# Kernel optimization log

Hardware: AMD Instinct MI355X
Metric: run time of the kernel (lower is better)

The kernel has to match this reference:

```python
import jax, jax.numpy as jnp
import numpy as np

V = 100000   # vocab (emb_size == stoich_size so all 8 branches index safely)
D = 256      # emb_dimension
S = 128      # stoich_dimension
H = 512      # hidden_size
B = 8192     # batch of skip-gram pairs
K = 32       # negative samples per pair
NUM_REGULAR = 60000  # num_regular_words


def _mlp(x, w1, b1, w2, b2):
    # Sequential(Linear(S,H), ReLU, Linear(H,D))
    return jax.nn.relu(x @ w1 + b1) @ w2 + b2


def setup_inputs() -> dict:
    key = jax.random.key(0)
    k = jax.random.split(key, 14)
    initrange = 1.0 / D
    return {
        "pos_u": jax.random.randint(k[0], (B,), 0, V),
        "pos_v": jax.random.randint(k[1], (B,), 0, V),
        "neg_v": jax.random.randint(k[2], (B, K), 0, V),
        "u_emb": jax.random.uniform(k[3], (V, D), jnp.float32, -initrange, initrange),
        "v_emb": jax.random.normal(k[4], (V, D), jnp.float32) * 0.01,
        "stoich": jax.random.uniform(k[5], (V, S), jnp.float32),
        "tw1": jax.random.normal(k[6], (S, H), jnp.float32) * 0.05,
        "tb1": jnp.zeros((H,), jnp.float32),
        "tw2": jax.random.normal(k[7], (H, D), jnp.float32) * 0.05,
        "tb2": jnp.zeros((D,), jnp.float32),
        "cw1": jax.random.normal(k[8], (S, H), jnp.float32) * 0.05,
        "cb1": jnp.zeros((H,), jnp.float32),
        "cw2": jax.random.normal(k[9], (H, D), jnp.float32) * 0.05,
        "cb2": jnp.zeros((D,), jnp.float32),
    }


def _masked_score(emb_u, emb_v, emb_neg_v, u_mask, v_mask, neg_v_mask):
    # pos: [B]
    pos = jnp.clip(jnp.sum(emb_u * emb_v, axis=1), -10.0, 10.0)
    pos = jnp.where(v_mask, 0.0, -jax.nn.log_sigmoid(pos))
    # neg: [B,K] = bmm(emb_neg_v [B,K,D], emb_u [B,D,1])
    neg = jnp.clip(jnp.einsum("bkd,bd->bk", emb_neg_v, emb_u), -10.0, 10.0)
    ls = jnp.where(neg_v_mask, 0.0, jax.nn.log_sigmoid(-neg))
    neg_score = -jnp.sum(ls, axis=1)
    return jnp.where(u_mask, 0.0, pos + neg_score)


def reference(pos_u, pos_v, neg_v, u_emb, v_emb, stoich,
              tw1, tb1, tw2, tb2, cw1, cb1, cw2, cb2):
    emb_u_w = u_emb[pos_u]                 # [B,D]
    emb_v_w = v_emb[pos_v]                 # [B,D]
    emb_neg_v_w = v_emb[neg_v]             # [B,K,D]
    emb_u_m = _mlp(stoich[pos_u], tw1, tb1, tw2, tb2)       # [B,D]
    emb_v_m = _mlp(stoich[pos_v], cw1, cb1, cw2, cb2)       # [B,D]
    emb_neg_v_m = _mlp(stoich[neg_v], cw1, cb1, cw2, cb2)   # [B,K,D]

    u_pairs = [(emb_u_w, pos_u >= NUM_REGULAR), (emb_u_m, pos_u < NUM_REGULAR)]
    v_pairs = [(emb_v_w, pos_v >= NUM_REGULAR), (emb_v_m, pos_v < NUM_REGULAR)]
    n_pairs = [(emb_neg_v_w, neg_v >= NUM_REGULAR), (emb_neg_v_m, neg_v < NUM_REGULAR)]

    total = jnp.zeros((B,), emb_u_w.dtype)
    for eu, um in u_pairs:
        for ev, vm in v_pairs:
            for env, nm in n_pairs:
                total = total + _masked_score(eu, ev, env, um, vm, nm)
    return jnp.mean(total)
```

## Files before the change

kernel.cpp:

```cpp
#include <hip/hip_runtime.h>
#include <hip/hip_bf16.h>
#include <math.h>

#define V_SIZE 100000
#define D_DIM  256
#define S_DIM  128
#define H_DIM  512
#define B_SIZE 8192
#define K_NEG  32
#define NR     60000
#define NMOD   (V_SIZE - NR)

#define TM     48
#define CBLK   834
#define UBLK   171
#define MC_PAD (CBLK * TM)
#define MU_PAD (UBLK * TM)
#define HPAD   516

typedef __attribute__((ext_vector_type(8))) short bf16x8;
typedef __attribute__((ext_vector_type(8))) unsigned short u16x8;
typedef __attribute__((ext_vector_type(4))) float f32x4;

static __device__ __forceinline__ short f2bf(float f) {
    unsigned u = __builtin_bit_cast(unsigned, f);
    unsigned r = (u + 0x7fffu + ((u >> 16) & 1u)) >> 16;
    return (short)r;
}
static __device__ __forceinline__ float bf2f(unsigned short h) {
    return __builtin_bit_cast(float, ((unsigned)h) << 16);
}


#define N_VC   (NR * D_DIM / 4)
#define N_CONV (MC_PAD * S_DIM / 4)
#define N_XU   (MU_PAD * S_DIM / 4)
#define N_TR   393216

__global__ __launch_bounds__(256) void prep_kernel(
    const float* __restrict__ stoich, const int* __restrict__ pos_u,
    const float* __restrict__ v_emb,
    const float* __restrict__ tw1, const float* __restrict__ cw1,
    const float* __restrict__ tw2, const float* __restrict__ cw2,
    short* __restrict__ vall,
    short* __restrict__ xc, short* __restrict__ xu,
    short* __restrict__ W1T_t, short* __restrict__ W1T_c,
    short* __restrict__ W2T_t, short* __restrict__ W2T_c)
{
    int t = blockIdx.x * 256 + threadIdx.x;
    if (t < N_VC) {
        int r  = t >> 6;
        int fr = t & 15;
        int wv = (t & 63) >> 4;
        const float* rp = v_emb + (size_t)r * D_DIM + wv * 64 + fr;
        short4 o;
        o.x = f2bf(rp[0]); o.y = f2bf(rp[16]); o.z = f2bf(rp[32]); o.w = f2bf(rp[48]);
        ((short4*)vall)[t] = o;
        return;
    }
    t -= N_VC;
    if (t < N_CONV + N_XU) {
        const bool cside = t < N_CONV;
        const int e    = (cside ? t : t - N_CONV) * 4;
        const int j0   = e & 7;
        const int lane = (e >> 3) & 63;
        const int ks   = (e >> 9) & 3;
        const int rt   = e >> 11;
        const int row  = rt * 16 + (lane & 15);
        const int k    = ks * 32 + (lane >> 4) * 8 + j0;
        short4 o = {0, 0, 0, 0};
        if (cside) {
            if (row < NMOD) {
                const float4 v = *(const float4*)(stoich + (size_t)(NR + row) * S_DIM + k);
                o.x = f2bf(v.x); o.y = f2bf(v.y); o.z = f2bf(v.z); o.w = f2bf(v.w);
            }
            ((short4*)xc)[t] = o;
        } else {
            if (row < B_SIZE) {
                int pu = pos_u[row];
                const float4 v = *(const float4*)(stoich + (size_t)pu * S_DIM + k);
                o.x = f2bf(v.x); o.y = f2bf(v.y); o.z = f2bf(v.z); o.w = f2bf(v.w);
            }
            ((short4*)xu)[t - N_CONV] = o;
        }
    } else {
        int t3 = t - (N_CONV + N_XU);
        if (t3 < 131072) {
            const float* src = (t3 < 65536) ? tw1 : cw1;
            short*       dst = (t3 < 65536) ? W1T_t : W1T_c;
            int t4 = t3 & 65535;
            int j = t4 & 7, lane = (t4 >> 3) & 63;
            int nt = (t4 >> 9) & 31, ks = (t4 >> 14) & 3;
            int k = ks * 32 + (lane >> 4) * 8 + j, n = nt * 16 + (lane & 15);
            dst[t4] = f2bf(src[(size_t)k * H_DIM + n]);
        } else {
            int t5 = t3 - 131072;
            const float* src = (t5 < 131072) ? tw2 : cw2;
            short*       dst = (t5 < 131072) ? W2T_t : W2T_c;
            int t4 = t5 & 131071;
            int j = t4 & 7, lane = (t4 >> 3) & 63;
            int nt = (t4 >> 9) & 15, ks = (t4 >> 13) & 15;
            int k = ks * 32 + (lane >> 4) * 8 + j, n = nt * 16 + (lane & 15);
            dst[t4] = f2bf(src[(size_t)k * D_DIM + n]);
        }
    }
}

__global__ __launch_bounds__(256, 3) void fused_mlp_kernel(
    const short* __restrict__ Xc,  const short* __restrict__ W1c,
    const float* __restrict__ b1c, const short* __restrict__ W2c,
    const float* __restrict__ b2c, short* __restrict__ outc,
    const short* __restrict__ Xu,  const short* __restrict__ W1u,
    const float* __restrict__ b1u, const short* __restrict__ W2u,
    const float* __restrict__ b2u, short* __restrict__ outu)
{
    __shared__ short sH[TM * HPAD];

    const int blk = blockIdx.x;
    const short *A, *W1T, *W2T; const float *b1, *b2; short* out;
    int m0, rtb;
    if (blk < CBLK) { A = Xc; W1T = W1c; b1 = b1c; W2T = W2c; b2 = b2c;
                      out = outc; m0 = blk * TM; rtb = blk * 3; }
    else            { A = Xu; W1T = W1u; b1 = b1u; W2T = W2u; b2 = b2u;
                      out = outu; m0 = (blk - CBLK) * TM; rtb = (blk - CBLK) * 3; }

    const int lane = threadIdx.x & 63;
    const int wv   = threadIdx.x >> 6;
    const int fr   = lane & 15;
    const int q    = lane >> 4;

    const short* Ap = A + (size_t)rtb * 2048 + lane * 8;
    bf16x8 af[4][3];
    #pragma unroll
    for (int ks = 0; ks < 4; ++ks)
        #pragma unroll
        for (int mi = 0; mi < 3; ++mi)
            af[ks][mi] = *(const bf16x8*)(Ap + mi * 2048 + ks * 512);

    #pragma unroll
    for (int half = 0; half < 2; ++half) {
        const int nt0 = wv * 8 + half * 4;
        const short* Bp = W1T + (size_t)nt0 * 512 + lane * 8;
        f32x4 acc[3][4] = {};
        #pragma unroll
        for (int ks = 0; ks < 4; ++ks) {
            bf16x8 bfr[4];
            #pragma unroll
            for (int ni = 0; ni < 4; ++ni)
                bfr[ni] = *(const bf16x8*)(Bp + ks * 16384 + ni * 512);
            #pragma unroll
            for (int mi = 0; mi < 3; ++mi)
                #pragma unroll
                for (int ni = 0; ni < 4; ++ni)
                    acc[mi][ni] = __builtin_amdgcn_mfma_f32_16x16x32_bf16(
                        af[ks][mi], bfr[ni], acc[mi][ni], 0, 0, 0);
        }
        #pragma unroll
        for (int ni = 0; ni < 4; ++ni) {
            int c = (nt0 + ni) * 16 + fr;
            float bv = b1[c];
            #pragma unroll
            for (int mi = 0; mi < 3; ++mi)
                #pragma unroll
                for (int r = 0; r < 4; ++r)
                    sH[(mi * 16 + q * 4 + r) * HPAD + c] =
                        f2bf(fmaxf(acc[mi][ni][r] + bv, 0.f));
        }
    }

    const short* Bp2 = W2T + (size_t)(wv * 4) * 512 + lane * 8;
    f32x4 acc2[3][4] = {};
    bf16x8 bA[4], bB[4], bC[4], bD[4], aA[3], aB[3];

    #define LOAD_B(ks, dst)                                                   \
        _Pragma("unroll")                                                     \
        for (int ni = 0; ni < 4; ++ni)                                        \
            dst[ni] = *(const bf16x8*)(Bp2 + (ks) * 8192 + ni * 512);
    #define LOAD_A(ks, dst)                                                   \
        _Pragma("unroll")                                                     \
        for (int mi = 0; mi < 3; ++mi) {                                      \
            const short* hp = &sH[(mi * 16 + fr) * HPAD + (ks) * 32 + q * 8]; \
            short4 lo = *(const short4*)hp;                                   \
            short4 hi = *(const short4*)(hp + 4);                             \
            bf16x8 v;                                                         \
            v[0] = lo.x; v[1] = lo.y; v[2] = lo.z; v[3] = lo.w;               \
            v[4] = hi.x; v[5] = hi.y; v[6] = hi.z; v[7] = hi.w;               \
            dst[mi] = v;                                                      \
        }

    LOAD_B(0, bA);
    LOAD_B(1, bB);
    LOAD_B(2, bC);
    __syncthreads();
    LOAD_A(0, aA);
    #pragma unroll
    for (int ks = 0; ks < 16; ++ks) {
        if (ks < 13) { LOAD_B(ks + 3, bD); }
        if (ks < 15) { LOAD_A(ks + 1, aB); }
        #pragma unroll
        for (int mi = 0; mi < 3; ++mi)
            #pragma unroll
            for (int ni = 0; ni < 4; ++ni)
                acc2[mi][ni] = __builtin_amdgcn_mfma_f32_16x16x32_bf16(
                    aA[mi], bA[ni], acc2[mi][ni], 0, 0, 0);
        if (ks < 15) {
            #pragma unroll
            for (int i = 0; i < 4; ++i) { bA[i] = bB[i]; bB[i] = bC[i]; bC[i] = bD[i]; }
            #pragma unroll
            for (int i = 0; i < 3; ++i) aA[i] = aB[i];
        }
    }
    #undef LOAD_A
    #undef LOAD_B

    float bv[4];
    #pragma unroll
    for (int ni = 0; ni < 4; ++ni)
        bv[ni] = b2[wv * 64 + ni * 16 + fr];
    #pragma unroll
    for (int mi = 0; mi < 3; ++mi)
        #pragma unroll
        for (int r = 0; r < 4; ++r) {
            int row = m0 + mi * 16 + q * 4 + r;
            short4 s;
            s.x = f2bf(acc2[mi][0][r] + bv[0]);
            s.y = f2bf(acc2[mi][1][r] + bv[1]);
            s.z = f2bf(acc2[mi][2][r] + bv[2]);
            s.w = f2bf(acc2[mi][3][r] + bv[3]);
            *(short4*)(out + (size_t)row * D_DIM + wv * 64 + fr * 4) = s;
        }
}

__device__ __forceinline__ float logsig_fast(float x) {
    float t = __expf(-fabsf(x));
    return fminf(x, 0.f) - __logf(1.f + t);
}
__device__ __forceinline__ float clip10(float x) {
    return fminf(fmaxf(x, -10.f), 10.f);
}

__global__ __launch_bounds__(256) void score_kernel(
    const int*   __restrict__ pos_u,
    const int*   __restrict__ pos_v,
    const int*   __restrict__ neg_v,
    const float* __restrict__ u_emb,
    const unsigned short* __restrict__ Vall,
    const unsigned short* __restrict__ Ubuf,
    float* __restrict__ partials)
{
    const int b    = blockIdx.x;
    const int lane = threadIdx.x & 63;
    const int wv   = threadIdx.x >> 6;
    const int g    = lane >> 4;
    const int l    = lane & 15;
    const int w64  = (l >> 2) * 64;
    const int s4   = (l & 3) * 4;

    const int* nv = neg_v + (size_t)b * K_NEG + wv * 8;
    int ix0 = nv[g];
    int ix1 = nv[4 + g];
    const unsigned short* r0p = Vall + (size_t)ix0 * D_DIM + l * 16;
    const unsigned short* r1p = Vall + (size_t)ix1 * D_DIM + l * 16;
    u16x8 r0a = *(const u16x8*)r0p;
    u16x8 r0b = *(const u16x8*)(r0p + 8);
    u16x8 r1a = *(const u16x8*)r1p;
    u16x8 r1b = *(const u16x8*)(r1p + 8);
    u16x8 rpa, rpb;
    if (wv == 0) {
        const unsigned short* rpp = Vall + (size_t)pos_v[b] * D_DIM + l * 16;
        rpa = *(const u16x8*)rpp;
        rpb = *(const u16x8*)(rpp + 8);
    }

    float euf[16];
    int pu = pos_u[b];
    if (pu < NR) {
        const float* eup = u_emb + (size_t)pu * D_DIM;
        #pragma unroll
        for (int n = 0; n < 4; ++n) {
            float4 v = *(const float4*)(eup + w64 + n * 16 + s4);
            euf[0 + n] = v.x; euf[4 + n] = v.y; euf[8 + n] = v.z; euf[12 + n] = v.w;
        }
    } else {
        const unsigned short* eup = Ubuf + (size_t)b * D_DIM + l * 16;
        u16x8 h0 = *(const u16x8*)eup;
        u16x8 h1 = *(const u16x8*)(eup + 8);
        #pragma unroll
        for (int i = 0; i < 8; ++i) { euf[i] = bf2f(h0[i]); euf[8 + i] = bf2f(h1[i]); }
    }

    float part = 0.f;

    float d0 = 0.f, d1 = 0.f;
    #pragma unroll
    for (int i = 0; i < 8; ++i) {
        d0 += euf[i] * bf2f(r0a[i]) + euf[8 + i] * bf2f(r0b[i]);
        d1 += euf[i] * bf2f(r1a[i]) + euf[8 + i] * bf2f(r1b[i]);
    }
    #pragma unroll
    for (int o = 1; o < 16; o <<= 1) {
        d0 += __shfl_xor(d0, o, 64);
        d1 += __shfl_xor(d1, o, 64);
    }
    part -= logsig_fast(-clip10(d0));
    part -= logsig_fast(-clip10(d1));

    if (wv == 0) {
        float dp = 0.f;
        #pragma unroll
        for (int i = 0; i < 8; ++i)
            dp += euf[i] * bf2f(rpa[i]) + euf[8 + i] * bf2f(rpb[i]);
        #pragma unroll
        for (int o = 1; o < 16; o <<= 1) dp += __shfl_xor(dp, o, 64);
        if (g == 0) part -= logsig_fast(clip10(dp));
    }

    float ws = part;
    #pragma unroll
    for (int o = 32; o; o >>= 1) ws += __shfl_xor(ws, o, 64);
    __shared__ float sp[4];
    if (lane == 0) sp[wv] = ws * 0.0625f;
    __syncthreads();
    if (threadIdx.x == 0)
        partials[b] = sp[0] + sp[1] + sp[2] + sp[3];
}

__global__ __launch_bounds__(256) void reduce_kernel(
    const float* __restrict__ partials, float* __restrict__ out)
{
    float s = 0.f;
    for (int i = threadIdx.x; i < B_SIZE; i += 256) s += partials[i];
    #pragma unroll
    for (int o = 32; o; o >>= 1) s += __shfl_xor(s, o, 64);
    __shared__ float sp[4];
    if ((threadIdx.x & 63) == 0) sp[threadIdx.x >> 6] = s;
    __syncthreads();
    if (threadIdx.x == 0)
        out[0] = (sp[0] + sp[1] + sp[2] + sp[3]) * (2.0f / (float)B_SIZE);
}

extern "C" void kernel_launch(void* const* d_in, const int* in_sizes, int n_in,
                              void* d_out, int out_size, void* d_ws, size_t ws_size,
                              hipStream_t stream) {
    const int*   pos_u  = (const int*)  d_in[0];
    const int*   pos_v  = (const int*)  d_in[1];
    const int*   neg_v  = (const int*)  d_in[2];
    const float* u_emb  = (const float*)d_in[3];
    const float* v_emb  = (const float*)d_in[4];
    const float* stoich = (const float*)d_in[5];
    const float* tw1    = (const float*)d_in[6];
    const float* tb1    = (const float*)d_in[7];
    const float* tw2    = (const float*)d_in[8];
    const float* tb2    = (const float*)d_in[9];
    const float* cw1    = (const float*)d_in[10];
    const float* cb1    = (const float*)d_in[11];
    const float* cw2    = (const float*)d_in[12];
    const float* cb2    = (const float*)d_in[13];
    float* out = (float*)d_out;

    char* ws = (char*)d_ws;
    short* Xbf   = (short*)(ws);
    short* Xu    = (short*)(ws + 10248192);
    short* W1T_t = (short*)(ws + 12349440);
    short* W1T_c = (short*)(ws + 12480512);
    short* W2T_t = (short*)(ws + 12611584);
    short* W2T_c = (short*)(ws + 12873728);
    short* Vall  = (short*)(ws + 13135872);
    short* Ubuf  = (short*)(ws + 64352256);
    float* parts = (float*)(ws + 68554752);
    short* tab_c = Vall + (size_t)NR * D_DIM;

    dim3 blk(256);

    prep_kernel<<<dim3((N_VC + N_CONV + N_XU + N_TR) / 256), blk, 0, stream>>>(
        stoich, pos_u, v_emb, tw1, cw1, tw2, cw2,
        Vall, Xbf, Xu, W1T_t, W1T_c, W2T_t, W2T_c);

    fused_mlp_kernel<<<dim3(CBLK + UBLK), blk, 0, stream>>>(
        Xbf, W1T_c, cb1, W2T_c, cb2, tab_c,
        Xu,  W1T_t, tb1, W2T_t, tb2, Ubuf);

    score_kernel<<<dim3(B_SIZE), blk, 0, stream>>>(
        pos_u, pos_v, neg_v, u_emb,
        (const unsigned short*)Vall, (const unsigned short*)Ubuf, parts);
    reduce_kernel<<<dim3(1), blk, 0, stream>>>(parts, out);
}
```

Before: 291.7 us.

## Software-pipeline first MLP GEMM weight loads and fuse final reduction into score kernel

```diff
diff --git a/kernel.cpp b/kernel.cpp
--- a/kernel.cpp
+++ b/kernel.cpp
@@ -45,9 +45,11 @@
     short* __restrict__ vall,
     short* __restrict__ xc, short* __restrict__ xu,
     short* __restrict__ W1T_t, short* __restrict__ W1T_c,
-    short* __restrict__ W2T_t, short* __restrict__ W2T_c)
+    short* __restrict__ W2T_t, short* __restrict__ W2T_c,
+    unsigned int* __restrict__ cnt)
 {
     int t = blockIdx.x * 256 + threadIdx.x;
+    if (t == 0) *cnt = 0u;
     if (t < N_VC) {
         int r  = t >> 6;
         int fr = t & 15;
@@ -129,7 +131,14 @@
     const int fr   = lane & 15;
     const int q    = lane >> 4;
 
-    const short* Ap = A + (size_t)rtb * 2048 + lane * 8;
+    float b1v[8];
+    #pragma unroll
+    for (int i = 0; i < 8; ++i)
+        b1v[i] = b1[(wv * 8 + i) * 16 + fr];
+
+    const short* Ap  = A + (size_t)rtb * 2048 + lane * 8;
+    const short* Bp0 = W1T + (size_t)(wv * 8) * 512 + lane * 8;
+    const short* Bp1 = W1T + (size_t)(wv * 8 + 4) * 512 + lane * 8;
     bf16x8 af[4][3];
     #pragma unroll
     for (int ks = 0; ks < 4; ++ks)
@@ -137,45 +146,65 @@
         for (int mi = 0; mi < 3; ++mi)
             af[ks][mi] = *(const bf16x8*)(Ap + mi * 2048 + ks * 512);
 
-    #pragma unroll
-    for (int half = 0; half < 2; ++half) {
-        const int nt0 = wv * 8 + half * 4;
-        const short* Bp = W1T + (size_t)nt0 * 512 + lane * 8;
+    bf16x8 bX[4], bY[4], bZ[4];
+    #define LOAD_B1(bp, ks, dst)                                              \
+        _Pragma("unroll")                                                     \
+        for (int ni = 0; ni < 4; ++ni)                                        \
+            dst[ni] = *(const bf16x8*)((bp) + (ks) * 16384 + ni * 512);
+    #define MFMA12(ks, bsrc, accv)                                            \
+        _Pragma("unroll")                                                     \
+        for (int mi = 0; mi < 3; ++mi)                                        \
+            _Pragma("unroll")                                                 \
+            for (int ni = 0; ni < 4; ++ni)                                    \
+                accv[mi][ni] = __builtin_amdgcn_mfma_f32_16x16x32_bf16(       \
+                    af[ks][mi], bsrc[ni], accv[mi][ni], 0, 0, 0);
+    #define EPI1(h, accv)                                                     \
+        _Pragma("unroll")                                                     \
+        for (int ni = 0; ni < 4; ++ni) {                                      \
+            int c = (wv * 8 + (h) * 4 + ni) * 16 + fr;                        \
+            float bv = b1v[(h) * 4 + ni];                                     \
+            _Pragma("unroll")                                                 \
+            for (int mi = 0; mi < 3; ++mi)                                    \
+                _Pragma("unroll")                                             \
+                for (int r = 0; r < 4; ++r)                                   \
+                    sH[(mi * 16 + q * 4 + r) * HPAD + c] =                    \
+                        f2bf(fmaxf(accv[mi][ni][r] + bv, 0.f));               \
+        }
+
+    LOAD_B1(Bp0, 0, bX);
+    LOAD_B1(Bp0, 1, bY);
+    {
         f32x4 acc[3][4] = {};
-        #pragma unroll
-        for (int ks = 0; ks < 4; ++ks) {
-            bf16x8 bfr[4];
-            #pragma unroll
-            for (int ni = 0; ni < 4; ++ni)
-                bfr[ni] = *(const bf16x8*)(Bp + ks * 16384 + ni * 512);
-            #pragma unroll
-            for (int mi = 0; mi < 3; ++mi)
-                #pragma unroll
-                for (int ni = 0; ni < 4; ++ni)
-                    acc[mi][ni] = __builtin_amdgcn_mfma_f32_16x16x32_bf16(
-                        af[ks][mi], bfr[ni], acc[mi][ni], 0, 0, 0);
-        }
-        #pragma unroll
-        for (int ni = 0; ni < 4; ++ni) {
-            int c = (nt0 + ni) * 16 + fr;
-            float bv = b1[c];
-            #pragma unroll
-            for (int mi = 0; mi < 3; ++mi)
-                #pragma unroll
-                for (int r = 0; r < 4; ++r)
-                    sH[(mi * 16 + q * 4 + r) * HPAD + c] =
-                        f2bf(fmaxf(acc[mi][ni][r] + bv, 0.f));
-        }
-    }
-
+        LOAD_B1(Bp0, 2, bZ);  MFMA12(0, bX, acc);
+        LOAD_B1(Bp0, 3, bX);  MFMA12(1, bY, acc);
+        LOAD_B1(Bp1, 0, bY);  MFMA12(2, bZ, acc);
+        LOAD_B1(Bp1, 1, bZ);  MFMA12(3, bX, acc);
+        EPI1(0, acc);
+    }
     const short* Bp2 = W2T + (size_t)(wv * 4) * 512 + lane * 8;
     f32x4 acc2[3][4] = {};
     bf16x8 bA[4], bB[4], bC[4], bD[4], aA[3], aB[3];
-
-    #define LOAD_B(ks, dst)                                                   \
+    #define LOAD_B2(ks, dst)                                                  \
         _Pragma("unroll")                                                     \
         for (int ni = 0; ni < 4; ++ni)                                        \
             dst[ni] = *(const bf16x8*)(Bp2 + (ks) * 8192 + ni * 512);
+    {
+        f32x4 acc[3][4] = {};
+        LOAD_B1(Bp1, 2, bX);  MFMA12(0, bY, acc);
+        LOAD_B1(Bp1, 3, bY);  MFMA12(1, bZ, acc);
+        MFMA12(2, bX, acc);
+        MFMA12(3, bY, acc);
+        LOAD_B2(0, bA);
+        LOAD_B2(1, bB);
+        LOAD_B2(2, bC);
+        EPI1(1, acc);
+    }
+    #undef LOAD_B1
+    #undef MFMA12
+    #undef EPI1
+
+    __syncthreads();
+
     #define LOAD_A(ks, dst)                                                   \
         _Pragma("unroll")                                                     \
         for (int mi = 0; mi < 3; ++mi) {                                      \
@@ -188,14 +217,10 @@
             dst[mi] = v;                                                      \
         }
 
-    LOAD_B(0, bA);
-    LOAD_B(1, bB);
-    LOAD_B(2, bC);
-    __syncthreads();
     LOAD_A(0, aA);
     #pragma unroll
     for (int ks = 0; ks < 16; ++ks) {
-        if (ks < 13) { LOAD_B(ks + 3, bD); }
+        if (ks < 13) { LOAD_B2(ks + 3, bD); }
         if (ks < 15) { LOAD_A(ks + 1, aB); }
         #pragma unroll
         for (int mi = 0; mi < 3; ++mi)
@@ -211,7 +236,7 @@
         }
     }
     #undef LOAD_A
-    #undef LOAD_B
+    #undef LOAD_B2
 
     float bv[4];
     #pragma unroll
@@ -246,7 +271,9 @@
     const float* __restrict__ u_emb,
     const unsigned short* __restrict__ Vall,
     const unsigned short* __restrict__ Ubuf,
-    float* __restrict__ partials)
+    float* __restrict__ partials,
+    unsigned int* __restrict__ cnt,
+    float* __restrict__ out)
 {
     const int b    = blockIdx.x;
     const int lane = threadIdx.x & 63;
@@ -319,24 +346,30 @@
     #pragma unroll
     for (int o = 32; o; o >>= 1) ws += __shfl_xor(ws, o, 64);
     __shared__ float sp[4];
+    __shared__ int lastFlag;
     if (lane == 0) sp[wv] = ws * 0.0625f;
     __syncthreads();
-    if (threadIdx.x == 0)
-        partials[b] = sp[0] + sp[1] + sp[2] + sp[3];
-}
-
-__global__ __launch_bounds__(256) void reduce_kernel(
-    const float* __restrict__ partials, float* __restrict__ out)
-{
-    float s = 0.f;
-    for (int i = threadIdx.x; i < B_SIZE; i += 256) s += partials[i];
-    #pragma unroll
-    for (int o = 32; o; o >>= 1) s += __shfl_xor(s, o, 64);
-    __shared__ float sp[4];
-    if ((threadIdx.x & 63) == 0) sp[threadIdx.x >> 6] = s;
+    if (threadIdx.x == 0) {
+        __hip_atomic_store(&partials[b], sp[0] + sp[1] + sp[2] + sp[3],
+                           __ATOMIC_RELEASE, __HIP_MEMORY_SCOPE_AGENT);
+        unsigned old = __hip_atomic_fetch_add(cnt, 1u, __ATOMIC_ACQ_REL,
+                                              __HIP_MEMORY_SCOPE_AGENT);
+        lastFlag = (old == (unsigned)(B_SIZE - 1));
+    }
     __syncthreads();
-    if (threadIdx.x == 0)
-        out[0] = (sp[0] + sp[1] + sp[2] + sp[3]) * (2.0f / (float)B_SIZE);
+    if (lastFlag) {
+        float s = 0.f;
+        for (int i = threadIdx.x; i < B_SIZE; i += 256)
+            s += __hip_atomic_load(&partials[i], __ATOMIC_RELAXED,
+                                   __HIP_MEMORY_SCOPE_AGENT);
+        #pragma unroll
+        for (int o = 32; o; o >>= 1) s += __shfl_xor(s, o, 64);
+        __shared__ float sr[4];
+        if (lane == 0) sr[wv] = s;
+        __syncthreads();
+        if (threadIdx.x == 0)
+            out[0] = (sr[0] + sr[1] + sr[2] + sr[3]) * (2.0f / (float)B_SIZE);
+    }
 }
 
 extern "C" void kernel_launch(void* const* d_in, const int* in_sizes, int n_in,
@@ -368,13 +401,14 @@
     short* Vall  = (short*)(ws + 13135872);
     short* Ubuf  = (short*)(ws + 64352256);
     float* parts = (float*)(ws + 68554752);
+    unsigned int* cnt = (unsigned int*)(ws + 68587520);
     short* tab_c = Vall + (size_t)NR * D_DIM;
 
     dim3 blk(256);
 
     prep_kernel<<<dim3((N_VC + N_CONV + N_XU + N_TR) / 256), blk, 0, stream>>>(
         stoich, pos_u, v_emb, tw1, cw1, tw2, cw2,
-        Vall, Xbf, Xu, W1T_t, W1T_c, W2T_t, W2T_c);
+        Vall, Xbf, Xu, W1T_t, W1T_c, W2T_t, W2T_c, cnt);
 
     fused_mlp_kernel<<<dim3(CBLK + UBLK), blk, 0, stream>>>(
         Xbf, W1T_c, cb1, W2T_c, cb2, tab_c,
@@ -382,6 +416,6 @@
 
     score_kernel<<<dim3(B_SIZE), blk, 0, stream>>>(
         pos_u, pos_v, neg_v, u_emb,
-        (const unsigned short*)Vall, (const unsigned short*)Ubuf, parts);
-    reduce_kernel<<<dim3(1), blk, 0, stream>>>(parts, out);
-}
+        (const unsigned short*)Vall, (const unsigned short*)Ubuf,
+        parts, cnt, out);
+}
```

After: 685.2 us. +134.9%, slower.
